# Kernel optimization log

Hardware: AMD Instinct MI355X
Metric: run time of the kernel (lower is better)

Reference implementation:

```python
import jax, jax.numpy as jnp
import numpy as np

VOCAB = 11322
EMB = 300
HID = 512
B, K, T = 64, 100, 20
NUM_QT = 84
NUM_ANS = 30000


def _lstm_layer(x, lens, w_ih, w_hh, b_ih, b_hh):
    """x: [N, T, in], lens: [N]. PyTorch gate order i,f,g,o.
    Returns (outputs [N, T, H], final hidden at t == len-1 [N, H])."""
    N = x.shape[0]
    H = w_hh.shape[1]
    x_t = jnp.swapaxes(x, 0, 1)  # [T, N, in]
    ts = jnp.arange(x.shape[1])

    def step(carry, inp):
        h, c = carry
        xt, t = inp
        gates = xt @ w_ih.T + h @ w_hh.T + (b_ih + b_hh)  # [N, 4H]
        i, f, g, o = jnp.split(gates, 4, axis=-1)
        c_new = jax.nn.sigmoid(f) * c + jax.nn.sigmoid(i) * jnp.tanh(g)
        h_new = jax.nn.sigmoid(o) * jnp.tanh(c_new)
        mask = (t < lens)[:, None]  # freeze state past each seq's length
        h = jnp.where(mask, h_new, h)
        c = jnp.where(mask, c_new, c)
        return (h, c), h

    init = (jnp.zeros((N, H), x.dtype), jnp.zeros((N, H), x.dtype))
    (h_fin, _), ys = jax.lax.scan(step, init, (x_t, ts))
    return jnp.swapaxes(ys, 0, 1), h_fin


def setup_inputs() -> dict:
    key = jax.random.key(0)
    ks = jax.random.split(key, 16)
    s = 1.0 / np.sqrt(HID)
    W_embed = jax.random.normal(ks[0], (VOCAB, EMB), jnp.float32) * 0.02
    W_embed = W_embed.at[0].set(0.0)  # padding_idx=0
    inp = {
        'encoder_output': jax.random.normal(ks[1], (B, HID), jnp.float32),
        'opt': jax.random.randint(ks[2], (B, K, T), 0, VOCAB),
        'opt_len': jax.random.randint(ks[3], (B, K), 1, T + 1),
        'qt_idx': jax.random.randint(ks[4], (B,), 0, NUM_QT),
        'opt_idx': jax.random.randint(ks[5], (B, K), 0, NUM_ANS),
        'W_embed': W_embed,
        'w_ih0': jax.random.uniform(ks[6], (4 * HID, EMB), jnp.float32, -s, s),
        'w_hh0': jax.random.uniform(ks[7], (4 * HID, HID), jnp.float32, -s, s),
        'b_ih0': jax.random.uniform(ks[8], (4 * HID,), jnp.float32, -s, s),
        'b_hh0': jax.random.uniform(ks[9], (4 * HID,), jnp.float32, -s, s),
        'w_ih1': jax.random.uniform(ks[10], (4 * HID, HID), jnp.float32, -s, s),
        'w_hh1': jax.random.uniform(ks[11], (4 * HID, HID), jnp.float32, -s, s),
        'b_ih1': jax.random.uniform(ks[12], (4 * HID,), jnp.float32, -s, s),
        'b_hh1': jax.random.uniform(ks[13], (4 * HID,), jnp.float32, -s, s),
        'relevance': jax.random.uniform(ks[14], (NUM_QT, NUM_ANS)) < 0.02,
    }
    return inp


def reference(encoder_output, opt, opt_len, qt_idx, opt_idx, W_embed,
              w_ih0, w_hh0, b_ih0, b_hh0, w_ih1, w_hh1, b_ih1, b_hh1,
              relevance):
    bsz, num_opt, max_len = opt.shape
    options = opt.reshape(-1, max_len)            # [B*K, T]
    lens = opt_len.reshape(-1)                    # [B*K]
    emb = W_embed[options] * (options != 0)[..., None].astype(W_embed.dtype)
    ys1, _ = _lstm_layer(emb, lens, w_ih0, w_hh0, b_ih0, b_hh0)
    _, h2 = _lstm_layer(ys1, lens, w_ih1, w_hh1, b_ih1, b_hh1)
    options_feat = h2.reshape(bsz, num_opt, HID)
    scores = jnp.einsum('bkh,bh->bk', options_feat, encoder_output)
    # vectorized replacement of the per-sample dict-lookup loop
    qt_score = relevance[qt_idx[:, None], opt_idx].astype(scores.dtype)
    return scores, qt_score
```

## Files before the change

kernel.cpp:

```cpp
#include <hip/hip_runtime.h>

#define NSEQ 6400
#define TMAX 20
#define EMB 300
#define EMBP 320
#define HID 512
#define KL0 832
#define KL1 1024
#define NQT 84
#define NANS 30000
#define RELN (NQT * NANS)

typedef __bf16 bf16x8 __attribute__((ext_vector_type(8)));
typedef float f32x4 __attribute__((ext_vector_type(4)));
typedef unsigned short u16;

__device__ __forceinline__ u16 f2bf(float f) {
  union { float f; unsigned int i; } v; v.f = f;
  unsigned int r = v.i + 0x7fffu + ((v.i >> 16) & 1u);
  return (u16)(r >> 16);
}

__global__ __launch_bounds__(320) void embed_kernel(
    const int* __restrict__ opt, const float* __restrict__ Wemb, u16* __restrict__ embT) {
  int n = blockIdx.x;
  int e = threadIdx.x;
#pragma unroll 4
  for (int t = 0; t < TMAX; ++t) {
    int tok = opt[n * TMAX + t];
    float v = 0.f;
    if (e < EMB && tok != 0) v = Wemb[(size_t)tok * EMB + e];
    embT[((size_t)t * NSEQ + n) * EMBP + e] = f2bf(v);
  }
}

__global__ void prep_w0(const float* __restrict__ wih, const float* __restrict__ whh,
                        u16* __restrict__ W) {
  for (int idx = blockIdx.x * blockDim.x + threadIdx.x; idx < 2048 * KL0;
       idx += gridDim.x * blockDim.x) {
    int o = idx / KL0, c = idx % KL0;
    float v;
    if (c < EMB) v = wih[o * EMB + c];
    else if (c < EMBP) v = 0.f;
    else v = whh[o * HID + (c - EMBP)];
    W[idx] = f2bf(v);
  }
}
__global__ void prep_w1(const float* __restrict__ wih, const float* __restrict__ whh,
                        u16* __restrict__ W) {
  for (int idx = blockIdx.x * blockDim.x + threadIdx.x; idx < 2048 * KL1;
       idx += gridDim.x * blockDim.x) {
    int o = idx / KL1, c = idx % KL1;
    float v = (c < HID) ? wih[o * HID + c] : whh[o * HID + (c - HID)];
    W[idx] = f2bf(v);
  }
}
__global__ void prep_bias(const float* __restrict__ a, const float* __restrict__ b,
                          float* __restrict__ o) {
  int i = blockIdx.x * blockDim.x + threadIdx.x;
  if (i < 2048) o[i] = a[i] + b[i];
}

__global__ __launch_bounds__(512) void lstm_step(
    const u16* __restrict__ segA0, int strideA0, int K0,
    const u16* __restrict__ segA1,
    const u16* __restrict__ Wcat, int Ktot, int nK,
    const float* __restrict__ biasc,
    u16* __restrict__ h_new, float* __restrict__ c_state,
    const float* __restrict__ hf_old, float* __restrict__ hf_new,
    const int* __restrict__ lens, int t) {
  __shared__ __align__(16) u16 Atile[3][128 * 32];
  __shared__ __align__(16) u16 Btile[3][128 * 32];
  const int tid = threadIdx.x;
  const int wave = tid >> 6, lane = tid & 63;
  const int l15 = lane & 15, l4 = lane >> 4;
  const int wr = wave >> 1, wc = wave & 1;

  const int orig = blockIdx.x;
  const int nid = (orig & 7) * 100 + (orig >> 3);
  const int rowBlk = (nid >> 4) * 128;
  const int hb = (nid & 15) * 32;

  const int jhi = lane >> 2;
  const int lrow = wave * 16 + jhi;
  const int srcslot = (lane & 3) ^ ((lrow >> 1) & 3);
  const int offA0 = (rowBlk + lrow) * strideA0 + srcslot * 8;
  const int offA1 = (rowBlk + lrow) * HID + srcslot * 8;
  const int gB = lrow >> 5, hB = lrow & 31;
  const int offB = (gB * HID + hb + hB) * Ktot + srcslot * 8;

  auto stage = [&](int sel, int ks) {
    const int kbase = ks * 32;
    const bool s1 = kbase >= K0;
    const u16* aPtr = s1 ? (segA1 + (kbase - K0) + offA1) : (segA0 + kbase + offA0);
    __builtin_amdgcn_global_load_lds(
        (const __attribute__((address_space(1))) void*)aPtr,
        (__attribute__((address_space(3))) void*)(&Atile[sel][wave * 512]),
        16, 0, 0);
    __builtin_amdgcn_global_load_lds(
        (const __attribute__((address_space(1))) void*)(Wcat + offB + kbase),
        (__attribute__((address_space(3))) void*)(&Btile[sel][wave * 512]),
        16, 0, 0);
  };

  f32x4 acc[2][4] = {};
  const int kx = (l4 ^ ((l15 >> 1) & 3)) * 8;

  auto compute = [&](int sel) {
    bf16x8 a[2], b[4];
#pragma unroll
    for (int m = 0; m < 2; ++m)
      a[m] = *(const bf16x8*)(&Atile[sel][(wr * 32 + m * 16 + l15) * 32 + kx]);
#pragma unroll
    for (int g = 0; g < 4; ++g)
      b[g] = *(const bf16x8*)(&Btile[sel][(g * 32 + wc * 16 + l15) * 32 + kx]);
    __builtin_amdgcn_s_setprio(1);
#pragma unroll
    for (int m = 0; m < 2; ++m)
#pragma unroll
      for (int g = 0; g < 4; ++g)
        acc[m][g] = __builtin_amdgcn_mfma_f32_16x16x32_bf16(a[m], b[g], acc[m][g], 0, 0, 0);
    __builtin_amdgcn_s_setprio(0);
  };

  stage(0, 0);
  stage(1, 1);
  int sel = 0, pre = 2;
  for (int ks = 0; ks < nK; ++ks) {
    if (ks + 2 < nK) {
      stage(pre, ks + 2);
      if (++pre == 3) pre = 0;
      asm volatile("s_waitcnt vmcnt(4)" ::: "memory");
    } else if (ks + 1 < nK) {
      asm volatile("s_waitcnt vmcnt(2)" ::: "memory");
    } else {
      asm volatile("s_waitcnt vmcnt(0)" ::: "memory");
    }
    __builtin_amdgcn_s_barrier();
    compute(sel);
    if (++sel == 3) sel = 0;
    if (ks + 1 < nK) __builtin_amdgcn_s_barrier();
  }

  const int u = hb + wc * 16 + l15;
  const float bi = biasc[u], bff = biasc[512 + u], bg = biasc[1024 + u], bo = biasc[1536 + u];
#pragma unroll
  for (int m = 0; m < 2; ++m) {
    const int rbase = rowBlk + wr * 32 + m * 16 + l4 * 4;
    const size_t cmi = (size_t)u * NSEQ + rbase;
    f32x4 co4 = *(const f32x4*)(c_state + cmi);
    int4 ln4 = *(const int4*)(lens + rbase);
    f32x4 ho4;
    if (hf_new) ho4 = *(const f32x4*)(hf_old + cmi);
    f32x4 cn4, hn4;
    u16 hstore[4];
#pragma unroll
    for (int jj = 0; jj < 4; ++jj) {
      const int r = rbase + jj;
      float ip = acc[m][0][jj] + bi;
      float fp = acc[m][1][jj] + bff;
      float gp = acc[m][2][jj] + bg;
      float op = acc[m][3][jj] + bo;
      float co = co4[jj];
      float si = 1.f / (1.f + __expf(-ip));
      float sf = 1.f / (1.f + __expf(-fp));
      float so = 1.f / (1.f + __expf(-op));
      float tg = tanhf(gp);
      float cn = sf * co + si * tg;
      float hn = so * tanhf(cn);
      int len = (jj == 0) ? ln4.x : (jj == 1) ? ln4.y : (jj == 2) ? ln4.z : ln4.w;
      bool act = t < len;
      cn4[jj] = act ? cn : co;
      hstore[jj] = act ? f2bf(hn) : segA1[(size_t)r * HID + u];
      if (hf_new) hn4[jj] = act ? hn : ho4[jj];
    }
    *(f32x4*)(c_state + cmi) = cn4;
    if (hf_new) *(f32x4*)(hf_new + cmi) = hn4;
#pragma unroll
    for (int jj = 0; jj < 4; ++jj)
      h_new[(size_t)(rbase + jj) * HID + u] = hstore[jj];
  }
}

__global__ __launch_bounds__(256) void scores_kernel(
    const float* __restrict__ h2cm, const float* __restrict__ enc, float* __restrict__ out) {
  int n = (blockIdx.x >> 1) * 256 + threadIdx.x;
  int uh = (blockIdx.x & 1) * 256;
  const float* ep = enc + (n / 100) * HID + uh;
  float s = 0.f;
#pragma unroll 8
  for (int u = 0; u < 256; ++u) s += h2cm[(size_t)(uh + u) * NSEQ + n] * ep[u];
  atomicAdd(&out[n], s);
}

__global__ void detect_kernel(const unsigned char* __restrict__ rel, int* __restrict__ flags) {
  int a = 0, bb = 0, z = 0;
  for (int i = blockIdx.x * blockDim.x + threadIdx.x; i < RELN; i += gridDim.x * blockDim.x) {
    if (rel[i]) {
      if (i & 3) a = 1; else z = 1;
      if (i & 4) bb = 1;
    }
  }
  if (a) atomicOr(&flags[0], 1);
  if (bb) atomicOr(&flags[1], 1);
  if (z) atomicOr(&flags[2], 1);
}

__global__ void qt_kernel(const void* __restrict__ rel, const int* __restrict__ qt_idx,
                          const int* __restrict__ opt_idx, const int* __restrict__ flags,
                          float* __restrict__ out) {
  int n = blockIdx.x * blockDim.x + threadIdx.x;
  if (n >= NSEQ) return;
  long long idx = (long long)qt_idx[n / 100] * NANS + opt_idx[n];
  int fa = flags[0], fb = flags[1], fz = flags[2];
  bool hit;
  if (fa && fz)       hit = ((const unsigned char*)rel)[idx] != 0;
  else if (fa)        hit = ((const float*)rel)[idx] != 0.f;
  else if (fb)        hit = ((const int*)rel)[idx] != 0;
  else                hit = ((const long long*)rel)[idx] != 0;
  out[NSEQ + n] = hit ? 1.f : 0.f;
}

extern "C" void kernel_launch(void* const* d_in, const int* in_sizes, int n_in,
                              void* d_out, int out_size, void* d_ws, size_t ws_size,
                              hipStream_t stream) {
  (void)in_sizes; (void)n_in; (void)out_size; (void)ws_size;
  const float* enc    = (const float*)d_in[0];
  const int*   opt    = (const int*)d_in[1];
  const int*   optlen = (const int*)d_in[2];
  const int*   qtidx  = (const int*)d_in[3];
  const int*   optidx = (const int*)d_in[4];
  const float* Wemb   = (const float*)d_in[5];
  const float* wih0   = (const float*)d_in[6];
  const float* whh0   = (const float*)d_in[7];
  const float* bih0   = (const float*)d_in[8];
  const float* bhh0   = (const float*)d_in[9];
  const float* wih1   = (const float*)d_in[10];
  const float* whh1   = (const float*)d_in[11];
  const float* bih1   = (const float*)d_in[12];
  const float* bhh1   = (const float*)d_in[13];
  const void*  rel    = d_in[14];
  float* out = (float*)d_out;

  char* ws = (char*)d_ws;
  size_t off = 0;
  auto alloc = [&](size_t bytes) -> void* {
    void* p = (void*)(ws + off);
    off += (bytes + 255) & ~(size_t)255;
    return p;
  };
  u16* embT   = (u16*)alloc((size_t)TMAX * NSEQ * EMBP * 2);
  u16* W0     = (u16*)alloc((size_t)2048 * KL0 * 2);
  u16* W1     = (u16*)alloc((size_t)2048 * KL1 * 2);
  float* bc0  = (float*)alloc(2048 * 4);
  float* bc1  = (float*)alloc(2048 * 4);
  u16* h0b[2] = { (u16*)alloc((size_t)NSEQ * HID * 2), (u16*)alloc((size_t)NSEQ * HID * 2) };
  u16* h1b[2] = { (u16*)alloc((size_t)NSEQ * HID * 2), (u16*)alloc((size_t)NSEQ * HID * 2) };
  float* c0   = (float*)alloc((size_t)NSEQ * HID * 4);
  float* c1   = (float*)alloc((size_t)NSEQ * HID * 4);
  float* hf[2] = { (float*)alloc((size_t)NSEQ * HID * 4), (float*)alloc((size_t)NSEQ * HID * 4) };
  int* flags  = (int*)alloc(16);

  hipMemsetAsync(h0b[0], 0, (size_t)NSEQ * HID * 2, stream);
  hipMemsetAsync(h1b[0], 0, (size_t)NSEQ * HID * 2, stream);
  hipMemsetAsync(c0, 0, (size_t)NSEQ * HID * 4, stream);
  hipMemsetAsync(c1, 0, (size_t)NSEQ * HID * 4, stream);
  hipMemsetAsync(hf[0], 0, (size_t)NSEQ * HID * 4, stream);
  hipMemsetAsync(flags, 0, 16, stream);
  hipMemsetAsync(out, 0, (size_t)NSEQ * 4, stream);

  embed_kernel<<<NSEQ, EMBP, 0, stream>>>(opt, Wemb, embT);
  prep_w0<<<512, 256, 0, stream>>>(wih0, whh0, W0);
  prep_w1<<<512, 256, 0, stream>>>(wih1, whh1, W1);
  prep_bias<<<8, 256, 0, stream>>>(bih0, bhh0, bc0);
  prep_bias<<<8, 256, 0, stream>>>(bih1, bhh1, bc1);
  detect_kernel<<<256, 256, 0, stream>>>((const unsigned char*)rel, flags);

  for (int t = 0; t < TMAX; ++t) {
    int cur = t & 1, nxt = cur ^ 1;
    lstm_step<<<800, 512, 0, stream>>>(
        embT + (size_t)t * NSEQ * EMBP, EMBP, EMBP,
        h0b[cur], W0, KL0, KL0 / 32, bc0,
        h0b[nxt], c0, nullptr, nullptr, optlen, t);
    lstm_step<<<800, 512, 0, stream>>>(
        h0b[nxt], HID, HID,
        h1b[cur], W1, KL1, KL1 / 32, bc1,
        h1b[nxt], c1, hf[cur], hf[nxt], optlen, t);
  }

  scores_kernel<<<50, 256, 0, stream>>>(hf[0], enc, out);
  qt_kernel<<<(NSEQ + 255) / 256, 256, 0, stream>>>(rel, qtidx, optidx, flags, out);
}
```

Baseline: 2.323 ms.

## Enlarge LSTM step GEMM tiles to 256x256 with ping-pong double buffering

```diff
diff --git a/kernel.cpp b/kernel.cpp
--- a/kernel.cpp
+++ b/kernel.cpp
@@ -61,124 +61,163 @@
   if (i < 2048) o[i] = a[i] + b[i];
 }
 
-__global__ __launch_bounds__(512) void lstm_step(
+__global__ __launch_bounds__(512, 2) void lstm_step(
     const u16* __restrict__ segA0, int strideA0, int K0,
     const u16* __restrict__ segA1,
-    const u16* __restrict__ Wcat, int Ktot, int nK,
+    const u16* __restrict__ Wcat, int Ktot, int nkt,
     const float* __restrict__ biasc,
     u16* __restrict__ h_new, float* __restrict__ c_state,
     const float* __restrict__ hf_old, float* __restrict__ hf_new,
     const int* __restrict__ lens, int t) {
-  __shared__ __align__(16) u16 Atile[3][128 * 32];
-  __shared__ __align__(16) u16 Btile[3][128 * 32];
+  __shared__ __align__(16) u16 Abuf[2][256 * 64];
+  __shared__ __align__(16) u16 Bbuf[2][256 * 64];
   const int tid = threadIdx.x;
   const int wave = tid >> 6, lane = tid & 63;
   const int l15 = lane & 15, l4 = lane >> 4;
-  const int wr = wave >> 1, wc = wave & 1;
+  const int mw = wave >> 1, nw = wave & 1;
 
   const int orig = blockIdx.x;
-  const int nid = (orig & 7) * 100 + (orig >> 3);
-  const int rowBlk = (nid >> 4) * 128;
-  const int hb = (nid & 15) * 32;
-
-  const int jhi = lane >> 2;
-  const int lrow = wave * 16 + jhi;
-  const int srcslot = (lane & 3) ^ ((lrow >> 1) & 3);
-  const int offA0 = (rowBlk + lrow) * strideA0 + srcslot * 8;
-  const int offA1 = (rowBlk + lrow) * HID + srcslot * 8;
-  const int gB = lrow >> 5, hB = lrow & 31;
-  const int offB = (gB * HID + hb + hB) * Ktot + srcslot * 8;
-
-  auto stage = [&](int sel, int ks) {
-    const int kbase = ks * 32;
+  const int wgid = (orig & 7) * 25 + (orig >> 3);
+  const int rowBlk = (wgid >> 3) * 256;
+  const int hblk = (wgid & 7) * 64;
+
+  const int srow = tid >> 3;
+  const int sslot = (tid & 7) ^ (srow & 7);
+
+  auto stageA = [&](int sel, int hb, int kt) {
+    const int kbase = kt * 64;
     const bool s1 = kbase >= K0;
-    const u16* aPtr = s1 ? (segA1 + (kbase - K0) + offA1) : (segA0 + kbase + offA0);
-    __builtin_amdgcn_global_load_lds(
-        (const __attribute__((address_space(1))) void*)aPtr,
-        (__attribute__((address_space(3))) void*)(&Atile[sel][wave * 512]),
-        16, 0, 0);
-    __builtin_amdgcn_global_load_lds(
-        (const __attribute__((address_space(1))) void*)(Wcat + offB + kbase),
-        (__attribute__((address_space(3))) void*)(&Btile[sel][wave * 512]),
-        16, 0, 0);
-  };
-
-  f32x4 acc[2][4] = {};
-  const int kx = (l4 ^ ((l15 >> 1) & 3)) * 8;
-
-  auto compute = [&](int sel) {
-    bf16x8 a[2], b[4];
-#pragma unroll
-    for (int m = 0; m < 2; ++m)
-      a[m] = *(const bf16x8*)(&Atile[sel][(wr * 32 + m * 16 + l15) * 32 + kx]);
-#pragma unroll
-    for (int g = 0; g < 4; ++g)
-      b[g] = *(const bf16x8*)(&Btile[sel][(g * 32 + wc * 16 + l15) * 32 + kx]);
+#pragma unroll
+    for (int i = 0; i < 2; ++i) {
+      int lrow = hb * 128 + i * 64 + srow;
+      int gr = rowBlk + lrow;
+      const u16* src = s1 ? (segA1 + (size_t)gr * HID + (kbase - K0) + sslot * 8)
+                          : (segA0 + (size_t)gr * strideA0 + kbase + sslot * 8);
+      __builtin_amdgcn_global_load_lds(
+          (const __attribute__((address_space(1))) void*)src,
+          (__attribute__((address_space(3))) void*)(&Abuf[sel][lrow * 64 + (tid & 7) * 8]),
+          16, 0, 0);
+    }
+  };
+  auto stageB = [&](int sel, int hb, int kt) {
+    const int kbase = kt * 64;
+#pragma unroll
+    for (int i = 0; i < 2; ++i) {
+      int lrow = hb * 128 + i * 64 + srow;
+      int g = hb * 2 + i;
+      const u16* src = Wcat + (size_t)(g * HID + hblk + srow) * Ktot + kbase + sslot * 8;
+      __builtin_amdgcn_global_load_lds(
+          (const __attribute__((address_space(1))) void*)src,
+          (__attribute__((address_space(3))) void*)(&Bbuf[sel][lrow * 64 + (tid & 7) * 8]),
+          16, 0, 0);
+    }
+  };
+
+  f32x4 acc[4][8] = {};
+  bf16x8 a[2][2], bLo[4][2], bHi[4][2];
+
+  auto rdA = [&](int sel, int mhalf) {
+#pragma unroll
+    for (int mf = 0; mf < 2; ++mf)
+#pragma unroll
+      for (int ks = 0; ks < 2; ++ks) {
+        int row = mw * 64 + mhalf * 32 + mf * 16 + l15;
+        int q = (ks * 4 + l4) ^ (row & 7);
+        a[mf][ks] = *(const bf16x8*)&Abuf[sel][row * 64 + q * 8];
+      }
+  };
+  auto rdB = [&](int sel, int nhalf, bf16x8 b[4][2]) {
+#pragma unroll
+    for (int f = 0; f < 4; ++f)
+#pragma unroll
+      for (int ks = 0; ks < 2; ++ks) {
+        int nf = nhalf * 4 + f;
+        int row = (nf >> 1) * 64 + nw * 32 + (nf & 1) * 16 + l15;
+        int q = (ks * 4 + l4) ^ (row & 7);
+        b[f][ks] = *(const bf16x8*)&Bbuf[sel][row * 64 + q * 8];
+      }
+  };
+  auto mma = [&](bf16x8 b[4][2], int mhalf, int nhalf) {
     __builtin_amdgcn_s_setprio(1);
 #pragma unroll
-    for (int m = 0; m < 2; ++m)
-#pragma unroll
-      for (int g = 0; g < 4; ++g)
-        acc[m][g] = __builtin_amdgcn_mfma_f32_16x16x32_bf16(a[m], b[g], acc[m][g], 0, 0, 0);
+    for (int mf = 0; mf < 2; ++mf)
+#pragma unroll
+      for (int f = 0; f < 4; ++f)
+#pragma unroll
+        for (int ks = 0; ks < 2; ++ks)
+          acc[mhalf * 2 + mf][nhalf * 4 + f] = __builtin_amdgcn_mfma_f32_16x16x32_bf16(
+              a[mf][ks], b[f][ks], acc[mhalf * 2 + mf][nhalf * 4 + f], 0, 0, 0);
     __builtin_amdgcn_s_setprio(0);
   };
 
-  stage(0, 0);
-  stage(1, 1);
-  int sel = 0, pre = 2;
-  for (int ks = 0; ks < nK; ++ks) {
-    if (ks + 2 < nK) {
-      stage(pre, ks + 2);
-      if (++pre == 3) pre = 0;
-      asm volatile("s_waitcnt vmcnt(4)" ::: "memory");
-    } else if (ks + 1 < nK) {
-      asm volatile("s_waitcnt vmcnt(2)" ::: "memory");
-    } else {
-      asm volatile("s_waitcnt vmcnt(0)" ::: "memory");
+  stageA(0, 0, 0); stageA(0, 1, 0); stageB(0, 0, 0); stageB(0, 1, 0);
+  asm volatile("s_waitcnt vmcnt(0)" ::: "memory");
+  __builtin_amdgcn_s_barrier();
+
+  for (int kt = 0; kt < nkt; ++kt) {
+    const int cur = kt & 1, nxt = cur ^ 1;
+    const bool pf = (kt + 1 < nkt);
+    rdA(cur, 0); rdB(cur, 0, bLo);
+    if (pf) stageA(nxt, 0, kt + 1);
+    __builtin_amdgcn_s_barrier();
+    mma(bLo, 0, 0);
+    __builtin_amdgcn_s_barrier();
+    rdB(cur, 1, bHi);
+    if (pf) stageA(nxt, 1, kt + 1);
+    __builtin_amdgcn_s_barrier();
+    mma(bHi, 0, 1);
+    __builtin_amdgcn_s_barrier();
+    rdA(cur, 1);
+    if (pf) stageB(nxt, 0, kt + 1);
+    __builtin_amdgcn_s_barrier();
+    mma(bHi, 1, 1);
+    __builtin_amdgcn_s_barrier();
+    if (pf) stageB(nxt, 1, kt + 1);
+    mma(bLo, 1, 0);
+    if (pf) asm volatile("s_waitcnt vmcnt(0)" ::: "memory");
+    __builtin_amdgcn_s_barrier();
+  }
+
+#pragma unroll
+  for (int hs = 0; hs < 2; ++hs) {
+    const int uu = hblk + nw * 32 + hs * 16 + l15;
+    const float bi = biasc[uu], bff = biasc[512 + uu];
+    const float bgg = biasc[1024 + uu], bo = biasc[1536 + uu];
+#pragma unroll
+    for (int m = 0; m < 4; ++m) {
+      const int rbase = rowBlk + mw * 64 + m * 16 + l4 * 4;
+      const size_t cmi = (size_t)uu * NSEQ + rbase;
+      f32x4 co4 = *(const f32x4*)(c_state + cmi);
+      int4 ln4 = *(const int4*)(lens + rbase);
+      f32x4 ho4;
+      if (hf_new) ho4 = *(const f32x4*)(hf_old + cmi);
+      f32x4 cn4, hn4;
+      u16 hstore[4];
+#pragma unroll
+      for (int jj = 0; jj < 4; ++jj) {
+        float ip = acc[m][hs][jj] + bi;
+        float fp = acc[m][2 + hs][jj] + bff;
+        float gp = acc[m][4 + hs][jj] + bgg;
+        float op = acc[m][6 + hs][jj] + bo;
+        float co = co4[jj];
+        float si = 1.f / (1.f + __expf(-ip));
+        float sf = 1.f / (1.f + __expf(-fp));
+        float so = 1.f / (1.f + __expf(-op));
+        float tg = tanhf(gp);
+        float cn = sf * co + si * tg;
+        float hn = so * tanhf(cn);
+        int len = (jj == 0) ? ln4.x : (jj == 1) ? ln4.y : (jj == 2) ? ln4.z : ln4.w;
+        bool act = t < len;
+        cn4[jj] = act ? cn : co;
+        hstore[jj] = act ? f2bf(hn) : segA1[(size_t)(rbase + jj) * HID + uu];
+        if (hf_new) hn4[jj] = act ? hn : ho4[jj];
+      }
+      *(f32x4*)(c_state + cmi) = cn4;
+      if (hf_new) *(f32x4*)(hf_new + cmi) = hn4;
+#pragma unroll
+      for (int jj = 0; jj < 4; ++jj)
+        h_new[(size_t)(rbase + jj) * HID + uu] = hstore[jj];
     }
-    __builtin_amdgcn_s_barrier();
-    compute(sel);
-    if (++sel == 3) sel = 0;
-    if (ks + 1 < nK) __builtin_amdgcn_s_barrier();
-  }
-
-  const int u = hb + wc * 16 + l15;
-  const float bi = biasc[u], bff = biasc[512 + u], bg = biasc[1024 + u], bo = biasc[1536 + u];
-#pragma unroll
-  for (int m = 0; m < 2; ++m) {
-    const int rbase = rowBlk + wr * 32 + m * 16 + l4 * 4;
-    const size_t cmi = (size_t)u * NSEQ + rbase;
-    f32x4 co4 = *(const f32x4*)(c_state + cmi);
-    int4 ln4 = *(const int4*)(lens + rbase);
-    f32x4 ho4;
-    if (hf_new) ho4 = *(const f32x4*)(hf_old + cmi);
-    f32x4 cn4, hn4;
-    u16 hstore[4];
-#pragma unroll
-    for (int jj = 0; jj < 4; ++jj) {
-      const int r = rbase + jj;
-      float ip = acc[m][0][jj] + bi;
-      float fp = acc[m][1][jj] + bff;
-      float gp = acc[m][2][jj] + bg;
-      float op = acc[m][3][jj] + bo;
-      float co = co4[jj];
-      float si = 1.f / (1.f + __expf(-ip));
-      float sf = 1.f / (1.f + __expf(-fp));
-      float so = 1.f / (1.f + __expf(-op));
-      float tg = tanhf(gp);
-      float cn = sf * co + si * tg;
-      float hn = so * tanhf(cn);
-      int len = (jj == 0) ? ln4.x : (jj == 1) ? ln4.y : (jj == 2) ? ln4.z : ln4.w;
-      bool act = t < len;
-      cn4[jj] = act ? cn : co;
-      hstore[jj] = act ? f2bf(hn) : segA1[(size_t)r * HID + u];
-      if (hf_new) hn4[jj] = act ? hn : ho4[jj];
-    }
-    *(f32x4*)(c_state + cmi) = cn4;
-    if (hf_new) *(f32x4*)(hf_new + cmi) = hn4;
-#pragma unroll
-    for (int jj = 0; jj < 4; ++jj)
-      h_new[(size_t)(rbase + jj) * HID + u] = hstore[jj];
   }
 }
 
@@ -278,13 +317,13 @@
 
   for (int t = 0; t < TMAX; ++t) {
     int cur = t & 1, nxt = cur ^ 1;
-    lstm_step<<<800, 512, 0, stream>>>(
+    lstm_step<<<200, 512, 0, stream>>>(
         embT + (size_t)t * NSEQ * EMBP, EMBP, EMBP,
-        h0b[cur], W0, KL0, KL0 / 32, bc0,
+        h0b[cur], W0, KL0, KL0 / 64, bc0,
         h0b[nxt], c0, nullptr, nullptr, optlen, t);
-    lstm_step<<<800, 512, 0, stream>>>(
+    lstm_step<<<200, 512, 0, stream>>>(
         h0b[nxt], HID, HID,
-        h1b[cur], W1, KL1, KL1 / 32, bc1,
+        h1b[cur], W1, KL1, KL1 / 64, bc1,
         h1b[nxt], c1, hf[cur], hf[nxt], optlen, t);
   }
 
```

New measurement: 2.139 ms. 1.09x faster.
